# Kernel tuning notes

Hardware: AMD Instinct MI355X
Metric: run time of the kernel (lower is better)

## Reference

```python
import jax, jax.numpy as jnp
import numpy as np

VOCAB = 32000
NUM_STATE = 256
NLABEL = 64
BATCH = 128
MAXLEN = 256
# transition init scale chosen so E[e^2]*S*a^2/3 ~= 1 -> per-step magnitude ~constant
TRANS_A = 0.208


def setup_inputs() -> dict:
    key = jax.random.key(0)
    k1, k2, k3, k4 = jax.random.split(key, 4)
    sentences = jax.random.randint(k1, (BATCH, MAXLEN), 0, VOCAB, dtype=jnp.int64)
    # original init: input.weight ~ U(0.5, 0.5) (constant 0.5). Use U(0.25, 0.75) so the
    # emission stays bounded away from 0 (it is divided by) while not being degenerate.
    emb = jax.random.uniform(k2, (VOCAB, NUM_STATE), minval=0.25, maxval=0.75, dtype=jnp.float32)
    transition = jax.random.uniform(k3, (NUM_STATE, NUM_STATE), minval=-TRANS_A, maxval=TRANS_A, dtype=jnp.float32)
    output = jax.random.uniform(k4, (NUM_STATE, NLABEL), minval=-0.5, maxval=0.5, dtype=jnp.float32)
    return {"sentences": sentences, "emb": emb, "transition": transition, "output": output}


def reference(sentences, emb, transition, output):
    # emission: [maxlen, batch, num_state]
    em = emb[sentences.T]

    def step_fwd(carry, e):  # carry: [B,S]
        nxt = jnp.einsum('ij,bj->bi', transition, carry) * e
        return nxt, nxt

    _, fw_rest = jax.lax.scan(step_fwd, em[0], em[1:])
    forwards = jnp.concatenate([em[:1], fw_rest], axis=0)  # [L,B,S]

    em_rev = em[::-1]

    def step_bwd(carry, e):  # uses transition^T
        nxt = jnp.einsum('ji,bj->bi', transition, carry) * e
        return nxt, nxt

    _, bw_rest = jax.lax.scan(step_bwd, em_rev[0], em_rev[1:])
    backwards = jnp.concatenate([em_rev[:1], bw_rest], axis=0)[::-1]  # time-aligned [L,B,S]

    expected_count = forwards * backwards / em
    score = jnp.einsum('lbs,sn->lbn', expected_count, output)
    return score.transpose(1, 0, 2)  # [batch, maxlen, nlabel]
```

## Files before the change

kernel.cpp:

```cpp
#include <hip/hip_runtime.h>
#include <hip/hip_bf16.h>


typedef _Float16 half8 __attribute__((ext_vector_type(8)));
typedef _Float16 half4 __attribute__((ext_vector_type(4)));
typedef float    f32x4 __attribute__((ext_vector_type(4)));
typedef unsigned long long u64;

#define LL 256
#define BB 128
#define SS 256
#define BT 16
#define RSTR8 67
#define RSTRO 65

static __device__ __forceinline__ f32x4 mfma16f(half8 a, half8 b, f32x4 c) {
  return __builtin_amdgcn_mfma_f32_16x16x32_f16(a, b, c, 0, 0, 0);
}

static __device__ __forceinline__ void lds_barrier() {
  __asm__ __volatile__("s_waitcnt lgkmcnt(0)\n\ts_barrier" ::: "memory");
}

static __device__ __forceinline__ u64 pack4(f32x4 v) {
  union { half4 h; u64 u; } x;
  x.h[0] = (_Float16)v[0];
  x.h[1] = (_Float16)v[1];
  x.h[2] = (_Float16)v[2];
  x.h[3] = (_Float16)v[3];
  return x.u;
}

static __device__ __forceinline__ half8 read_frag_s(const u64* plane, int row,
                                                    int kt, int q, int stride8) {
  const int o = row * stride8 + kt * 8 + q * 2;
  union { u64 u[2]; half8 v; } x;
  x.u[0] = plane[o];
  x.u[1] = plane[o + 1];
  return x.v;
}

__global__ __launch_bounds__(1024, 4)
void hmm_chain(const int* __restrict__ sent, const float* __restrict__ emb,
               const float* __restrict__ T, _Float16* __restrict__ fwh,
               _Float16* __restrict__ gh)
{
  __shared__ u64 s_carry[2][BT * RSTR8];
  __shared__ u64 v_pl[2][BT * RSTR8];
  __shared__ int s_tok[BT * 257];

  const int tid  = threadIdx.x;
  const int lane = tid & 63;
  const int w    = tid >> 6;
  const int m    = lane & 15;
  const int q    = lane >> 4;

  const int  bid = blockIdx.x;
  const bool fwd = (bid < 8);
  const int  bg0 = (fwd ? bid : bid - 8) * BT;
  _Float16* const obuf = fwd ? fwh : gh;
  const int  st  = 16 * w + 4 * q;

  for (int idx = tid; idx < BT * LL; idx += 1024) {
    int bb = idx >> 8, l2 = idx & 255;
    s_tok[bb * 257 + l2] = sent[(bg0 + bb) * LL + l2];
  }
  __syncthreads();

  half8 a_hi[8];
#pragma unroll
  for (int kt = 0; kt < 8; ++kt) {
    const int r0 = 16 * w + m;
    const int kb = 32 * kt + 8 * q;
    float v[8];
    if (fwd) {
      f32x4 f0 = *(const f32x4*)(T + r0 * 256 + kb);
      f32x4 f1 = *(const f32x4*)(T + r0 * 256 + kb + 4);
#pragma unroll
      for (int j = 0; j < 4; ++j) { v[j] = f0[j]; v[4 + j] = f1[j]; }
    } else {
#pragma unroll
      for (int j = 0; j < 8; ++j) v[j] = T[(kb + j) * 256 + r0];
    }
    half8 hi;
#pragma unroll
    for (int j = 0; j < 8; ++j) hi[j] = (_Float16)v[j];
    a_hi[kt] = hi;
  }

  const int l0 = fwd ? 0 : (LL - 1);
  {
    const int tok0 = s_tok[m * 257 + l0];
    f32x4 e0 = *(const f32x4*)(emb + (size_t)tok0 * 256 + st);
    u64 pc = pack4(e0);
    s_carry[0][m * RSTR8 + 4 * w + q] = pc;
    if (!fwd) {
      f32x4 one = 1.0f;
      v_pl[0][m * RSTR8 + 4 * w + q] = pack4(one);
    }
  }

  f32x4 em_pref;
  {
    const int l1 = fwd ? 1 : (LL - 2);
    const int tok1 = s_tok[m * 257 + l1];
    em_pref = *(const f32x4*)(emb + (size_t)tok1 * 256 + st);
  }
  __syncthreads();

  for (int s = 1; s < LL; ++s) {
    const int lp = fwd ? (s - 1) : (LL - s);
    const int rb = (s - 1) & 1, wb = s & 1;

    const u64* pr = &s_carry[rb][0];
    half8 bfr[8];
#pragma unroll
    for (int kt = 0; kt < 8; ++kt)
      bfr[kt] = read_frag_s(pr, m, kt, q, RSTR8);

    const u64* op = fwd ? &s_carry[rb][0] : &v_pl[rb][0];
    u64 ov = op[w * RSTR8 + lane];

    f32x4 em_now = em_pref;
    {
      const int ln = fwd ? (s + 1 < LL ? s + 1 : LL - 1)
                         : ((LL - 2) - s > 0 ? (LL - 2) - s : 0);
      const int tokn = s_tok[m * 257 + ln];
      em_pref = *(const f32x4*)(emb + (size_t)tokn * 256 + st);
    }

    f32x4 hh = 0.0f;
#pragma unroll
    for (int kt = 0; kt < 8; ++kt)
      hh = mfma16f(a_hi[kt], bfr[kt], hh);
    f32x4 v  = hh;
    f32x4 cn = v * em_now;

    u64 p0 = pack4(cn);
    s_carry[wb][m * RSTR8 + 4 * w + q] = p0;
    if (!fwd)
      v_pl[wb][m * RSTR8 + 4 * w + q] = pack4(v);

    *(u64*)(obuf + ((size_t)lp * BB + bg0 + w) * SS + lane * 4) = ov;

    lds_barrier();
  }

  {
    const int lp = fwd ? (LL - 1) : 0;
    const u64* op = fwd ? &s_carry[1][0] : &v_pl[1][0];
    u64 ov = op[w * RSTR8 + lane];
    *(u64*)(obuf + ((size_t)lp * BB + bg0 + w) * SS + lane * 4) = ov;
  }
}

__global__ __launch_bounds__(256, 2)
void hmm_score(const _Float16* __restrict__ fwh, const _Float16* __restrict__ gh,
               const float* __restrict__ outm, float* __restrict__ score)
{
  __shared__ u64 p_pl[64 * RSTR8];
  __shared__ u64 o_pl[64 * RSTRO];

  const int tid  = threadIdx.x;
  const int lane = tid & 63;
  const int w    = tid >> 6;
  const int rh   = w >> 1;
  const int np   = w & 1;
  const int m    = lane & 15;
  const int q    = lane >> 4;
  const int R0   = blockIdx.x * 64;

  {
    _Float16* o_h = (_Float16*)o_pl;
    for (int i = tid; i < 4096; i += 256) {
      f32x4 v = *(const f32x4*)(outm + i * 4);
      int k = i >> 4, n0 = (i & 15) * 4;
#pragma unroll
      for (int r = 0; r < 4; ++r)
        o_h[(n0 + r) * (RSTRO * 4) + k] = (_Float16)v[r];
    }
  }

  for (int idx = tid; idx < 64 * 64; idx += 256) {
    int row = idx >> 6, c = idx & 63;
    union { u64 u; half4 h; } a, b, p;
    a.u = *(const u64*)(fwh + (size_t)(R0 + row) * 256 + c * 4);
    b.u = *(const u64*)(gh  + (size_t)(R0 + row) * 256 + c * 4);
    p.h = a.h * b.h;
    p_pl[row * RSTR8 + c] = p.u;
  }
  lds_barrier();

  f32x4 acc[2][2];
#pragma unroll
  for (int j = 0; j < 2; ++j)
#pragma unroll
    for (int jn = 0; jn < 2; ++jn) acc[j][jn] = 0.0f;

#pragma unroll
  for (int kt = 0; kt < 8; ++kt) {
    half8 of[2];
#pragma unroll
    for (int jn = 0; jn < 2; ++jn)
      of[jn] = read_frag_s(o_pl, 16 * (2 * np + jn) + m, kt, q, RSTRO);
#pragma unroll
    for (int j = 0; j < 2; ++j) {
      half8 pf = read_frag_s(p_pl, 32 * rh + 16 * j + m, kt, q, RSTR8);
#pragma unroll
      for (int jn = 0; jn < 2; ++jn)
        acc[j][jn] = mfma16f(pf, of[jn], acc[j][jn]);
    }
  }

#pragma unroll
  for (int j = 0; j < 2; ++j) {
#pragma unroll
    for (int jn = 0; jn < 2; ++jn) {
#pragma unroll
      for (int r = 0; r < 4; ++r) {
        int row = R0 + 32 * rh + 16 * j + 4 * q + r;
        int l = row >> 7, b = row & 127;
        score[(size_t)b * 16384 + l * 64 + 16 * (2 * np + jn) + m] = acc[j][jn][r];
      }
    }
  }
}

extern "C" void kernel_launch(void* const* d_in, const int* in_sizes, int n_in,
                              void* d_out, int out_size, void* d_ws, size_t ws_size,
                              hipStream_t stream) {
  (void)in_sizes; (void)n_in; (void)out_size; (void)ws_size;
  const int*   sent = (const int*)d_in[0];
  const float* emb  = (const float*)d_in[1];
  const float* T    = (const float*)d_in[2];
  const float* outm = (const float*)d_in[3];
  _Float16* fwh = (_Float16*)d_ws;
  _Float16* gh  = fwh + (size_t)LL * BB * SS;

  hmm_chain<<<16, 1024, 0, stream>>>(sent, emb, T, fwh, gh);
  hmm_score<<<512, 256, 0, stream>>>(fwh, gh, outm, (float*)d_out);
}
```

Measured before the change: 263.2 us.

## Split each chain block's batch into two independent 8-row halves

Each chain block's 16 batch rows are now split into two independent 8-row groups with separate carry buffers. Each step issues two MFMA chains, with rows duplicated across the 16-row tile, so the two dependent chains can interleave. The global store of the previous step's state moves after the barrier. The change doubles MFMA and LDS read work per step and uses half of each MFMA's output rows, in exchange for more instruction-level parallelism on the latency-bound serial recurrence.

Result: slower. 430.0 us (+63.4%).

```diff
diff --git a/kernel.cpp b/kernel.cpp
--- a/kernel.cpp
+++ b/kernel.cpp
@@ -10,7 +10,6 @@
 #define LL 256
 #define BB 128
 #define SS 256
-#define BT 16
 #define RSTR8 67
 #define RSTRO 65
 
@@ -45,23 +44,26 @@
                const float* __restrict__ T, _Float16* __restrict__ fwh,
                _Float16* __restrict__ gh)
 {
-  __shared__ u64 s_carry[2][BT * RSTR8];
-  __shared__ u64 v_pl[2][BT * RSTR8];
-  __shared__ int s_tok[BT * 257];
+  __shared__ u64 cA[2][8 * RSTR8];
+  __shared__ u64 cB[2][8 * RSTR8];
+  __shared__ u64 vA[2][8 * RSTR8];
+  __shared__ u64 vB[2][8 * RSTR8];
+  __shared__ int s_tok[16 * 257];
 
   const int tid  = threadIdx.x;
   const int lane = tid & 63;
   const int w    = tid >> 6;
   const int m    = lane & 15;
+  const int mr   = m & 7;
   const int q    = lane >> 4;
 
   const int  bid = blockIdx.x;
   const bool fwd = (bid < 8);
-  const int  bg0 = (fwd ? bid : bid - 8) * BT;
+  const int  bg0 = (fwd ? bid : bid - 8) * 16;
   _Float16* const obuf = fwd ? fwh : gh;
   const int  st  = 16 * w + 4 * q;
 
-  for (int idx = tid; idx < BT * LL; idx += 1024) {
+  for (int idx = tid; idx < 16 * LL; idx += 1024) {
     int bb = idx >> 8, l2 = idx & 255;
     s_tok[bb * 257 + l2] = sent[(bg0 + bb) * LL + l2];
   }
@@ -90,21 +92,27 @@
 
   const int l0 = fwd ? 0 : (LL - 1);
   {
-    const int tok0 = s_tok[m * 257 + l0];
-    f32x4 e0 = *(const f32x4*)(emb + (size_t)tok0 * 256 + st);
-    u64 pc = pack4(e0);
-    s_carry[0][m * RSTR8 + 4 * w + q] = pc;
-    if (!fwd) {
-      f32x4 one = 1.0f;
-      v_pl[0][m * RSTR8 + 4 * w + q] = pack4(one);
-    }
-  }
-
-  f32x4 em_pref;
+    const int tkA = s_tok[mr * 257 + l0];
+    const int tkB = s_tok[(8 + mr) * 257 + l0];
+    f32x4 eA = *(const f32x4*)(emb + (size_t)tkA * 256 + st);
+    f32x4 eB = *(const f32x4*)(emb + (size_t)tkB * 256 + st);
+    if (m < 8) {
+      cA[0][m * RSTR8 + 4 * w + q] = pack4(eA);
+      cB[0][m * RSTR8 + 4 * w + q] = pack4(eB);
+      if (!fwd) {
+        f32x4 one = 1.0f;
+        u64 pone = pack4(one);
+        vA[0][m * RSTR8 + 4 * w + q] = pone;
+        vB[0][m * RSTR8 + 4 * w + q] = pone;
+      }
+    }
+  }
+
+  f32x4 em_prefA, em_prefB;
   {
     const int l1 = fwd ? 1 : (LL - 2);
-    const int tok1 = s_tok[m * 257 + l1];
-    em_pref = *(const f32x4*)(emb + (size_t)tok1 * 256 + st);
+    em_prefA = *(const f32x4*)(emb + (size_t)s_tok[mr * 257 + l1] * 256 + st);
+    em_prefB = *(const f32x4*)(emb + (size_t)s_tok[(8 + mr) * 257 + l1] * 256 + st);
   }
   __syncthreads();
 
@@ -112,45 +120,65 @@
     const int lp = fwd ? (s - 1) : (LL - s);
     const int rb = (s - 1) & 1, wb = s & 1;
 
-    const u64* pr = &s_carry[rb][0];
-    half8 bfr[8];
-#pragma unroll
-    for (int kt = 0; kt < 8; ++kt)
-      bfr[kt] = read_frag_s(pr, m, kt, q, RSTR8);
-
-    const u64* op = fwd ? &s_carry[rb][0] : &v_pl[rb][0];
-    u64 ov = op[w * RSTR8 + lane];
-
-    f32x4 em_now = em_pref;
+    u64 ovv;
+    {
+      const u64* opA = fwd ? &cA[rb][0] : &vA[rb][0];
+      const u64* opB = fwd ? &cB[rb][0] : &vB[rb][0];
+      ovv = (w < 8) ? opA[w * RSTR8 + lane] : opB[(w - 8) * RSTR8 + lane];
+    }
+
+    f32x4 emA = em_prefA, emB = em_prefB;
     {
       const int ln = fwd ? (s + 1 < LL ? s + 1 : LL - 1)
                          : ((LL - 2) - s > 0 ? (LL - 2) - s : 0);
-      const int tokn = s_tok[m * 257 + ln];
-      em_pref = *(const f32x4*)(emb + (size_t)tokn * 256 + st);
-    }
-
-    f32x4 hh = 0.0f;
-#pragma unroll
-    for (int kt = 0; kt < 8; ++kt)
-      hh = mfma16f(a_hi[kt], bfr[kt], hh);
-    f32x4 v  = hh;
-    f32x4 cn = v * em_now;
-
-    u64 p0 = pack4(cn);
-    s_carry[wb][m * RSTR8 + 4 * w + q] = p0;
-    if (!fwd)
-      v_pl[wb][m * RSTR8 + 4 * w + q] = pack4(v);
-
-    *(u64*)(obuf + ((size_t)lp * BB + bg0 + w) * SS + lane * 4) = ov;
+      em_prefA = *(const f32x4*)(emb + (size_t)s_tok[mr * 257 + ln] * 256 + st);
+      em_prefB = *(const f32x4*)(emb + (size_t)s_tok[(8 + mr) * 257 + ln] * 256 + st);
+    }
+
+    {
+      const u64* pr = &cA[rb][0];
+      half8 bfr[8];
+#pragma unroll
+      for (int kt = 0; kt < 8; ++kt)
+        bfr[kt] = read_frag_s(pr, mr, kt, q, RSTR8);
+      f32x4 hh = 0.0f;
+#pragma unroll
+      for (int kt = 0; kt < 8; ++kt)
+        hh = mfma16f(a_hi[kt], bfr[kt], hh);
+      f32x4 cn = hh * emA;
+      if (m < 8) {
+        cA[wb][m * RSTR8 + 4 * w + q] = pack4(cn);
+        if (!fwd) vA[wb][m * RSTR8 + 4 * w + q] = pack4(hh);
+      }
+    }
+
+    {
+      const u64* pr = &cB[rb][0];
+      half8 bfr[8];
+#pragma unroll
+      for (int kt = 0; kt < 8; ++kt)
+        bfr[kt] = read_frag_s(pr, mr, kt, q, RSTR8);
+      f32x4 hh = 0.0f;
+#pragma unroll
+      for (int kt = 0; kt < 8; ++kt)
+        hh = mfma16f(a_hi[kt], bfr[kt], hh);
+      f32x4 cn = hh * emB;
+      if (m < 8) {
+        cB[wb][m * RSTR8 + 4 * w + q] = pack4(cn);
+        if (!fwd) vB[wb][m * RSTR8 + 4 * w + q] = pack4(hh);
+      }
+    }
 
     lds_barrier();
+    *(u64*)(obuf + ((size_t)lp * BB + bg0 + w) * SS + lane * 4) = ovv;
   }
 
   {
     const int lp = fwd ? (LL - 1) : 0;
-    const u64* op = fwd ? &s_carry[1][0] : &v_pl[1][0];
-    u64 ov = op[w * RSTR8 + lane];
-    *(u64*)(obuf + ((size_t)lp * BB + bg0 + w) * SS + lane * 4) = ov;
+    const u64* opA = fwd ? &cA[1][0] : &vA[1][0];
+    const u64* opB = fwd ? &cB[1][0] : &vB[1][0];
+    u64 ovv = (w < 8) ? opA[w * RSTR8 + lane] : opB[(w - 8) * RSTR8 + lane];
+    *(u64*)(obuf + ((size_t)lp * BB + bg0 + w) * SS + lane * 4) = ovv;
   }
 }
 
```
